# Optimization experiments

Hardware: AMD Instinct MI355X
Metric: run time of the kernel (lower is better)

Reference implementation:

```python
import jax, jax.numpy as jnp
import numpy as np

TOP_K = 8
NUM_EXPERTS = 32
CAPACITY = 1024


def setup_inputs() -> dict:
    key = jax.random.key(0)
    k1, k2, k3, k4 = jax.random.split(key, 4)
    B, S, H, E, F = 2, 1024, 1024, NUM_EXPERTS, 768
    return {
        "hidden_states": jax.random.normal(k1, (B, S, H), dtype=jnp.float32),
        "gate_weight": jax.random.normal(k2, (E, H), dtype=jnp.float32) * 0.02,
        "gate_up_proj": jax.random.normal(k3, (E, 2 * F, H), dtype=jnp.float32) * 0.02,
        "down_proj": jax.random.normal(k4, (E, H, F), dtype=jnp.float32) * 0.02,
    }


def reference(hidden_states, gate_weight, gate_up_proj, down_proj):
    B, S, H = hidden_states.shape
    E = gate_weight.shape[0]
    N = B * S
    x = hidden_states.reshape(N, H)

    # Router: fp32 softmax, top-k, renormalize (norm_topk_prob=True)
    logits = x @ gate_weight.T                                   # [N, E]
    probs = jax.nn.softmax(logits.astype(jnp.float32), axis=-1)
    topw, topi = jax.lax.top_k(probs, TOP_K)                     # [N, K]
    topw = topw / topw.sum(-1, keepdims=True)
    topw = topw.astype(x.dtype)

    # Flatten token-slot view (matches repeat_interleave ordering)
    flat_e = topi.reshape(-1)                                    # [N*K] int
    flat_w = topw.reshape(-1)                                    # [N*K]
    flat_x = jnp.repeat(x, TOP_K, axis=0)                        # [N*K, H]

    # Position of each slot within its expert (stable order, like stable argsort)
    oh = jax.nn.one_hot(flat_e, E, dtype=jnp.int32)              # [N*K, E]
    pos = (jnp.cumsum(oh, axis=0) * oh).sum(-1) - 1              # [N*K]

    # Dispatch into per-expert buffers [E, C, H]; grouped GEMMs; gather back
    buf = jnp.zeros((E, CAPACITY, H), x.dtype).at[flat_e, pos].set(flat_x, mode="drop")
    gu = jnp.einsum("ech,efh->ecf", buf, gate_up_proj)           # [E, C, 2F]
    gate, up = jnp.split(gu, 2, axis=-1)
    h = jax.nn.silu(gate) * up                                   # [E, C, F]
    eo = jnp.einsum("ecf,ehf->ech", h, down_proj)                # [E, C, H]
    tok_out = eo.at[flat_e, pos].get(mode="fill", fill_value=0)  # [N*K, H]

    out = (tok_out * flat_w[:, None]).reshape(N, TOP_K, H).sum(1)
    return out.reshape(B, S, H)
```

## Files before the change

kernel.cpp:

```cpp
#include <hip/hip_runtime.h>
#include <stdint.h>
#include <math.h>

#define NTOK  2048
#define HDIM  1024
#define FDIM  768
#define NEXP  32
#define TOPK  8
#define CAP   1024

typedef __attribute__((ext_vector_type(8))) short short8;
typedef __attribute__((ext_vector_type(4))) float f32x4;

__device__ __forceinline__ short f2bf(float f) {
  union { float f; uint32_t u; } c; c.f = f;
  uint32_t u = c.u;
  u += 0x7fffu + ((u >> 16) & 1u);
  return (short)(u >> 16);
}

__device__ __forceinline__ short8 pack8(float4 a, float4 b) {
  short8 r;
  r[0] = f2bf(a.x); r[1] = f2bf(a.y); r[2] = f2bf(a.z); r[3] = f2bf(a.w);
  r[4] = f2bf(b.x); r[5] = f2bf(b.y); r[6] = f2bf(b.z); r[7] = f2bf(b.w);
  return r;
}

__device__ __forceinline__ void gload16(const short* g, short* l) {
  __builtin_amdgcn_global_load_lds(
      (__attribute__((address_space(1))) uint32_t*)g,
      (__attribute__((address_space(3))) uint32_t*)l, 16, 0, 0);
}

__global__ __launch_bounds__(256) void cvt_kern(
    const float* __restrict__ gup, const float* __restrict__ dwn,
    short* __restrict__ gupb, short* __restrict__ dwnb) {
  const size_t NG8 = (size_t)NEXP * 2 * FDIM * HDIM / 8;
  const size_t ND8 = (size_t)NEXP * HDIM * FDIM / 8;
  const size_t tid = (size_t)blockIdx.x * 256 + threadIdx.x;
  const size_t stride = (size_t)gridDim.x * 256;
  for (size_t i = tid; i < NG8; i += stride) {
    const float4 a = *(const float4*)(gup + i * 8);
    const float4 b = *(const float4*)(gup + i * 8 + 4);
    *(short8*)(gupb + i * 8) = pack8(a, b);
  }
  for (size_t i = tid; i < ND8; i += stride) {
    const float4 a = *(const float4*)(dwn + i * 8);
    const float4 b = *(const float4*)(dwn + i * 8 + 4);
    *(short8*)(dwnb + i * 8) = pack8(a, b);
  }
}

__global__ __launch_bounds__(256) void router_kern(
    const float* __restrict__ x, const float* __restrict__ gw,
    int* __restrict__ cnt, int* __restrict__ slot_tok,
    float* __restrict__ slot_w, short* __restrict__ xb) {
  const int n0 = blockIdx.x * 8;
  const int t  = threadIdx.x;
  __shared__ float ls[8][32];

  const int e = t >> 3;
  const int j = t & 7;
  float acc[8];
#pragma unroll
  for (int i = 0; i < 8; ++i) acc[i] = 0.f;
  const float* gwe = gw + (size_t)e * HDIM;
  for (int i = 0; i < 128; ++i) {
    const int k = j + 8 * i;
    const float gv = gwe[k];
#pragma unroll
    for (int tok = 0; tok < 8; ++tok)
      acc[tok] += gv * x[(size_t)(n0 + tok) * HDIM + k];
  }
#pragma unroll
  for (int tok = 0; tok < 8; ++tok) {
    float v = acc[tok];
    v += __shfl_xor(v, 1); v += __shfl_xor(v, 2); v += __shfl_xor(v, 4);
    if (j == 0) ls[tok][e] = v;
  }
  __syncthreads();

  if (t < 8) {
    const int n = n0 + t;
    float lv[32];
#pragma unroll
    for (int i = 0; i < 32; ++i) lv[i] = ls[t][i];
    int   idx[TOPK];
    float val[TOPK];
    for (int kk = 0; kk < TOPK; ++kk) {
      float best = -INFINITY; int bi = 0;
      for (int i = 0; i < 32; ++i)
        if (lv[i] > best) { best = lv[i]; bi = i; }
      val[kk] = best; idx[kk] = bi; lv[bi] = -INFINITY;
    }
    const float m = val[0];
    float w[TOPK]; float wsum = 0.f;
    for (int kk = 0; kk < TOPK; ++kk) { w[kk] = __expf(val[kk] - m); wsum += w[kk]; }
    const float inv = 1.f / wsum;
    for (int kk = 0; kk < TOPK; ++kk) {
      const int ee = idx[kk];
      const int pos = atomicAdd(&cnt[ee], 1);
      if (pos < CAP) {
        slot_tok[ee * CAP + pos] = n * TOPK + kk;
        slot_w[ee * CAP + pos]   = w[kk] * inv;
      }
    }
  }

  const size_t base = (size_t)n0 * HDIM;
  for (int i = t; i < 8 * HDIM; i += 256)
    xb[base + i] = f2bf(x[base + i]);
}

__global__ __launch_bounds__(256) void gemm1_kern(
    const short* __restrict__ xb, const short* __restrict__ gupb,
    const int* __restrict__ cnt, const int* __restrict__ slot_tok,
    short* __restrict__ hbuf) {
  const int id  = blockIdx.x;
  const int xcd = id & 7;
  const int idx = id >> 3;
  const int e   = xcd + 8 * (idx / 96);
  const int w96 = idx % 96;
  const int f0  = (w96 % 12) * 64;
  const int r0  = (w96 / 12) * 128;

  const int mcnt = min(cnt[e], CAP);
  if (r0 >= mcnt) return;

  __shared__ short As[2][128 * 32];
  __shared__ short Bg[2][64 * 32];
  __shared__ short Bu[2][64 * 32];

  const int t = threadIdx.x;
  const int wave = t >> 6, lane = t & 63;

  const int la0 = wave * 128 + lane;
  const int la1 = la0 + 64;
  const int arow0 = la0 >> 2, aseg0 = la0 & 3;
  const int arow1 = la1 >> 2, aseg1 = la1 & 3;
  int tok0 = 0, tok1 = 0;
  if (r0 + arow0 < mcnt) tok0 = slot_tok[e * CAP + r0 + arow0] >> 3;
  if (r0 + arow1 < mcnt) tok1 = slot_tok[e * CAP + r0 + arow1] >> 3;
  const short* aSrc0 = xb + (size_t)tok0 * HDIM + aseg0 * 8;
  const short* aSrc1 = xb + (size_t)tok1 * HDIM + aseg1 * 8;

  const int brow = t >> 2, bseg = t & 3;
  const short* gSrc = gupb + ((size_t)e * 1536 + f0 + brow) * HDIM + bseg * 8;
  const short* uSrc = gupb + ((size_t)e * 1536 + 768 + f0 + brow) * HDIM + bseg * 8;

  const int wm = (wave & 1) * 64, wf = (wave >> 1) * 32;
  const int lrow = lane & 15, lk = (lane >> 4) * 8;

  f32x4 accg[4][2], accu[4][2];
#pragma unroll
  for (int a = 0; a < 4; ++a)
#pragma unroll
    for (int b = 0; b < 2; ++b) {
      accg[a][b] = (f32x4){0.f, 0.f, 0.f, 0.f};
      accu[a][b] = (f32x4){0.f, 0.f, 0.f, 0.f};
    }

  auto STAGE = [&](int b, int kb) {
    gload16(aSrc0 + kb, &As[b][wave * 1024]);
    gload16(aSrc1 + kb, &As[b][wave * 1024 + 512]);
    gload16(gSrc + kb,  &Bg[b][wave * 512]);
    gload16(uSrc + kb,  &Bu[b][wave * 512]);
  };

  auto COMPUTE = [&](int b) {
    short8 af[4], bg[2], bu[2];
#pragma unroll
    for (int mt = 0; mt < 4; ++mt)
      af[mt] = *(const short8*)&As[b][(wm + mt * 16 + lrow) * 32 + lk];
#pragma unroll
    for (int nt = 0; nt < 2; ++nt) {
      bg[nt] = *(const short8*)&Bg[b][(wf + nt * 16 + lrow) * 32 + lk];
      bu[nt] = *(const short8*)&Bu[b][(wf + nt * 16 + lrow) * 32 + lk];
    }
#pragma unroll
    for (int mt = 0; mt < 4; ++mt)
#pragma unroll
      for (int nt = 0; nt < 2; ++nt) {
        accg[mt][nt] = __builtin_amdgcn_mfma_f32_16x16x32_bf16(af[mt], bg[nt], accg[mt][nt], 0, 0, 0);
        accu[mt][nt] = __builtin_amdgcn_mfma_f32_16x16x32_bf16(af[mt], bu[nt], accu[mt][nt], 0, 0, 0);
      }
  };

  STAGE(0, 0);
  __syncthreads();
  int cur = 0;
  for (int kb = 32; kb < HDIM; kb += 32) {
    STAGE(cur ^ 1, kb);
    COMPUTE(cur);
    __syncthreads();
    cur ^= 1;
  }
  COMPUTE(cur);

#pragma unroll
  for (int mt = 0; mt < 4; ++mt)
#pragma unroll
    for (int rr = 0; rr < 4; ++rr) {
      const int pos = r0 + wm + mt * 16 + (lane >> 4) * 4 + rr;
      if (pos < mcnt) {
#pragma unroll
        for (int nt = 0; nt < 2; ++nt) {
          const float g = accg[mt][nt][rr];
          const float u = accu[mt][nt][rr];
          const float hv = (g / (1.f + __expf(-g))) * u;
          hbuf[((size_t)e * CAP + pos) * FDIM + f0 + wf + nt * 16 + (lane & 15)] = f2bf(hv);
        }
      }
    }
}

__global__ __launch_bounds__(256) void gemm2_kern(
    const short* __restrict__ hbuf, const short* __restrict__ dwnb,
    const int* __restrict__ cnt, const int* __restrict__ slot_tok,
    const float* __restrict__ slot_w, float* __restrict__ slot_out) {
  const int id  = blockIdx.x;
  const int xcd = id & 7;
  const int idx = id >> 3;
  const int e   = xcd + 8 * (idx >> 6);
  const int w64 = idx & 63;
  const int n0  = (w64 & 7) * 128;
  const int r0  = (w64 >> 3) * 128;

  const int mcnt = min(cnt[e], CAP);
  if (r0 >= mcnt) return;

  __shared__ short As[2][128 * 32];
  __shared__ short Bs[2][128 * 32];

  const int t = threadIdx.x;
  const int wave = t >> 6, lane = t & 63;

  const int l0 = wave * 128 + lane;
  const int l1 = l0 + 64;
  const int ar0 = l0 >> 2, as0 = l0 & 3;
  const int ar1 = l1 >> 2, as1 = l1 & 3;
  const short* aSrc0 = hbuf + ((size_t)e * CAP + r0 + ar0) * FDIM + as0 * 8;
  const short* aSrc1 = hbuf + ((size_t)e * CAP + r0 + ar1) * FDIM + as1 * 8;
  const short* bSrc0 = dwnb + ((size_t)e * HDIM + n0 + ar0) * FDIM + as0 * 8;
  const short* bSrc1 = dwnb + ((size_t)e * HDIM + n0 + ar1) * FDIM + as1 * 8;

  const int wm = (wave & 1) * 64, wn = (wave >> 1) * 64;
  const int lrow = lane & 15, lk = (lane >> 4) * 8;

  f32x4 acc[4][4];
#pragma unroll
  for (int a = 0; a < 4; ++a)
#pragma unroll
    for (int b = 0; b < 4; ++b) acc[a][b] = (f32x4){0.f, 0.f, 0.f, 0.f};

  auto STAGE = [&](int b, int kb) {
    gload16(aSrc0 + kb, &As[b][wave * 1024]);
    gload16(aSrc1 + kb, &As[b][wave * 1024 + 512]);
    gload16(bSrc0 + kb, &Bs[b][wave * 1024]);
    gload16(bSrc1 + kb, &Bs[b][wave * 1024 + 512]);
  };

  auto COMPUTE = [&](int b) {
    short8 af[4], bf[4];
#pragma unroll
    for (int i = 0; i < 4; ++i) {
      af[i] = *(const short8*)&As[b][(wm + i * 16 + lrow) * 32 + lk];
      bf[i] = *(const short8*)&Bs[b][(wn + i * 16 + lrow) * 32 + lk];
    }
#pragma unroll
    for (int mt = 0; mt < 4; ++mt)
#pragma unroll
      for (int nt = 0; nt < 4; ++nt)
        acc[mt][nt] = __builtin_amdgcn_mfma_f32_16x16x32_bf16(af[mt], bf[nt], acc[mt][nt], 0, 0, 0);
  };

  STAGE(0, 0);
  __syncthreads();
  int cur = 0;
  for (int kb = 32; kb < FDIM; kb += 32) {
    STAGE(cur ^ 1, kb);
    COMPUTE(cur);
    __syncthreads();
    cur ^= 1;
  }
  COMPUTE(cur);

#pragma unroll
  for (int mt = 0; mt < 4; ++mt)
#pragma unroll
    for (int rr = 0; rr < 4; ++rr) {
      const int pos = r0 + wm + mt * 16 + (lane >> 4) * 4 + rr;
      if (pos < mcnt) {
        const int s = slot_tok[e * CAP + pos];
        const float w = slot_w[e * CAP + pos];
#pragma unroll
        for (int nt = 0; nt < 4; ++nt)
          slot_out[(size_t)s * HDIM + n0 + wn + nt * 16 + (lane & 15)] = w * acc[mt][nt][rr];
      }
    }
}

__global__ __launch_bounds__(256) void gather_kern(
    const float* __restrict__ so, float* __restrict__ out) {
  const int n = blockIdx.x;
  const int c = threadIdx.x * 4;
  float4 a = make_float4(0.f, 0.f, 0.f, 0.f);
#pragma unroll
  for (int k = 0; k < TOPK; ++k) {
    const float4 v = *(const float4*)&so[((size_t)(n * TOPK + k)) * HDIM + c];
    a.x += v.x; a.y += v.y; a.z += v.z; a.w += v.w;
  }
  *(float4*)&out[(size_t)n * HDIM + c] = a;
}

extern "C" void kernel_launch(void* const* d_in, const int* in_sizes, int n_in,
                              void* d_out, int out_size, void* d_ws, size_t ws_size,
                              hipStream_t stream) {
  const float* x   = (const float*)d_in[0];
  const float* gw  = (const float*)d_in[1];
  const float* gup = (const float*)d_in[2];
  const float* dwn = (const float*)d_in[3];
  float* out = (float*)d_out;

  char* ws = (char*)d_ws;
  int*   cnt      = (int*)(ws + 0);
  int*   slot_tok = (int*)(ws + 1024);
  float* slot_w   = (float*)(ws + 1024 + 131072);
  short* xb       = (short*)(ws + 524288);
  short* hbuf     = (short*)(ws + 4718592);
  short* gupb     = (short*)(ws + 55050240);
  short* dwnb     = (short*)(ws + 155713536);
  float* slot_out = (float*)(ws + 206045184);

  hipMemsetAsync(cnt, 0, 1024, stream);
  router_kern<<<NTOK / 8, 256, 0, stream>>>(x, gw, cnt, slot_tok, slot_w, xb);
  cvt_kern<<<4096, 256, 0, stream>>>(gup, dwn, gupb, dwnb);
  gemm1_kern<<<3072, 256, 0, stream>>>(xb, gupb, cnt, slot_tok, hbuf);
  gemm2_kern<<<2048, 256, 0, stream>>>(hbuf, dwnb, cnt, slot_tok, slot_w, slot_out);
  gather_kern<<<NTOK, 256, 0, stream>>>(slot_out, out);
}
```

Before: 603.7 us.

## Fuse fp32-to-bf16 weight conversion into grouped GEMM tile loads

Removes the separate kernel that converted all expert weights to bf16 each call. The GEMMs instead load fp32 weight tiles into registers and pack them to bf16 when writing shared memory, overlapped with the MFMA compute on the other buffer. This avoids a full-weight write and re-read pass, at the cost of reading twice as many weight bytes per tile, repeated across row blocks. It also replaces asynchronous LDS-direct loads with register-staged loads.

```diff
diff --git a/kernel.cpp b/kernel.cpp
--- a/kernel.cpp
+++ b/kernel.cpp
@@ -30,25 +30,6 @@
   __builtin_amdgcn_global_load_lds(
       (__attribute__((address_space(1))) uint32_t*)g,
       (__attribute__((address_space(3))) uint32_t*)l, 16, 0, 0);
-}
-
-__global__ __launch_bounds__(256) void cvt_kern(
-    const float* __restrict__ gup, const float* __restrict__ dwn,
-    short* __restrict__ gupb, short* __restrict__ dwnb) {
-  const size_t NG8 = (size_t)NEXP * 2 * FDIM * HDIM / 8;
-  const size_t ND8 = (size_t)NEXP * HDIM * FDIM / 8;
-  const size_t tid = (size_t)blockIdx.x * 256 + threadIdx.x;
-  const size_t stride = (size_t)gridDim.x * 256;
-  for (size_t i = tid; i < NG8; i += stride) {
-    const float4 a = *(const float4*)(gup + i * 8);
-    const float4 b = *(const float4*)(gup + i * 8 + 4);
-    *(short8*)(gupb + i * 8) = pack8(a, b);
-  }
-  for (size_t i = tid; i < ND8; i += stride) {
-    const float4 a = *(const float4*)(dwn + i * 8);
-    const float4 b = *(const float4*)(dwn + i * 8 + 4);
-    *(short8*)(dwnb + i * 8) = pack8(a, b);
-  }
 }
 
 __global__ __launch_bounds__(256) void router_kern(
@@ -113,7 +94,7 @@
 }
 
 __global__ __launch_bounds__(256) void gemm1_kern(
-    const short* __restrict__ xb, const short* __restrict__ gupb,
+    const short* __restrict__ xb, const float* __restrict__ gup,
     const int* __restrict__ cnt, const int* __restrict__ slot_tok,
     short* __restrict__ hbuf) {
   const int id  = blockIdx.x;
@@ -145,8 +126,8 @@
   const short* aSrc1 = xb + (size_t)tok1 * HDIM + aseg1 * 8;
 
   const int brow = t >> 2, bseg = t & 3;
-  const short* gSrc = gupb + ((size_t)e * 1536 + f0 + brow) * HDIM + bseg * 8;
-  const short* uSrc = gupb + ((size_t)e * 1536 + 768 + f0 + brow) * HDIM + bseg * 8;
+  const float* gSrcF = gup + ((size_t)(e * 1536 + f0 + brow)) * HDIM + bseg * 8;
+  const float* uSrcF = gup + ((size_t)(e * 1536 + 768 + f0 + brow)) * HDIM + bseg * 8;
 
   const int wm = (wave & 1) * 64, wf = (wave >> 1) * 32;
   const int lrow = lane & 15, lk = (lane >> 4) * 8;
@@ -160,11 +141,20 @@
       accu[a][b] = (f32x4){0.f, 0.f, 0.f, 0.f};
     }
 
-  auto STAGE = [&](int b, int kb) {
+  float4 g0, g1, u0, u1;
+
+  auto STAGE_LOAD = [&](int b, int kb) {
     gload16(aSrc0 + kb, &As[b][wave * 1024]);
     gload16(aSrc1 + kb, &As[b][wave * 1024 + 512]);
-    gload16(gSrc + kb,  &Bg[b][wave * 512]);
-    gload16(uSrc + kb,  &Bu[b][wave * 512]);
+    g0 = *(const float4*)(gSrcF + kb);
+    g1 = *(const float4*)(gSrcF + kb + 4);
+    u0 = *(const float4*)(uSrcF + kb);
+    u1 = *(const float4*)(uSrcF + kb + 4);
+  };
+
+  auto STAGE_WRITE = [&](int b) {
+    *(short8*)&Bg[b][t * 8] = pack8(g0, g1);
+    *(short8*)&Bu[b][t * 8] = pack8(u0, u1);
   };
 
   auto COMPUTE = [&](int b) {
@@ -186,12 +176,14 @@
       }
   };
 
-  STAGE(0, 0);
+  STAGE_LOAD(0, 0);
+  STAGE_WRITE(0);
   __syncthreads();
   int cur = 0;
   for (int kb = 32; kb < HDIM; kb += 32) {
-    STAGE(cur ^ 1, kb);
+    STAGE_LOAD(cur ^ 1, kb);
     COMPUTE(cur);
+    STAGE_WRITE(cur ^ 1);
     __syncthreads();
     cur ^= 1;
   }
@@ -215,7 +207,7 @@
 }
 
 __global__ __launch_bounds__(256) void gemm2_kern(
-    const short* __restrict__ hbuf, const short* __restrict__ dwnb,
+    const short* __restrict__ hbuf, const float* __restrict__ dwn,
     const int* __restrict__ cnt, const int* __restrict__ slot_tok,
     const float* __restrict__ slot_w, float* __restrict__ slot_out) {
   const int id  = blockIdx.x;
@@ -241,8 +233,8 @@
   const int ar1 = l1 >> 2, as1 = l1 & 3;
   const short* aSrc0 = hbuf + ((size_t)e * CAP + r0 + ar0) * FDIM + as0 * 8;
   const short* aSrc1 = hbuf + ((size_t)e * CAP + r0 + ar1) * FDIM + as1 * 8;
-  const short* bSrc0 = dwnb + ((size_t)e * HDIM + n0 + ar0) * FDIM + as0 * 8;
-  const short* bSrc1 = dwnb + ((size_t)e * HDIM + n0 + ar1) * FDIM + as1 * 8;
+  const float* bSrcF0 = dwn + ((size_t)(e * HDIM + n0 + ar0)) * FDIM + as0 * 8;
+  const float* bSrcF1 = dwn + ((size_t)(e * HDIM + n0 + ar1)) * FDIM + as1 * 8;
 
   const int wm = (wave & 1) * 64, wn = (wave >> 1) * 64;
   const int lrow = lane & 15, lk = (lane >> 4) * 8;
@@ -253,11 +245,20 @@
 #pragma unroll
     for (int b = 0; b < 4; ++b) acc[a][b] = (f32x4){0.f, 0.f, 0.f, 0.f};
 
-  auto STAGE = [&](int b, int kb) {
+  float4 b00, b01, b10, b11;
+
+  auto STAGE_LOAD = [&](int b, int kb) {
     gload16(aSrc0 + kb, &As[b][wave * 1024]);
     gload16(aSrc1 + kb, &As[b][wave * 1024 + 512]);
-    gload16(bSrc0 + kb, &Bs[b][wave * 1024]);
-    gload16(bSrc1 + kb, &Bs[b][wave * 1024 + 512]);
+    b00 = *(const float4*)(bSrcF0 + kb);
+    b01 = *(const float4*)(bSrcF0 + kb + 4);
+    b10 = *(const float4*)(bSrcF1 + kb);
+    b11 = *(const float4*)(bSrcF1 + kb + 4);
+  };
+
+  auto STAGE_WRITE = [&](int b) {
+    *(short8*)&Bs[b][l0 * 8] = pack8(b00, b01);
+    *(short8*)&Bs[b][l1 * 8] = pack8(b10, b11);
   };
 
   auto COMPUTE = [&](int b) {
@@ -274,12 +275,14 @@
         acc[mt][nt] = __builtin_amdgcn_mfma_f32_16x16x32_bf16(af[mt], bf[nt], acc[mt][nt], 0, 0, 0);
   };
 
-  STAGE(0, 0);
+  STAGE_LOAD(0, 0);
+  STAGE_WRITE(0);
   __syncthreads();
   int cur = 0;
   for (int kb = 32; kb < FDIM; kb += 32) {
-    STAGE(cur ^ 1, kb);
+    STAGE_LOAD(cur ^ 1, kb);
     COMPUTE(cur);
+    STAGE_WRITE(cur ^ 1);
     __syncthreads();
     cur ^= 1;
   }
@@ -328,14 +331,11 @@
   float* slot_w   = (float*)(ws + 1024 + 131072);
   short* xb       = (short*)(ws + 524288);
   short* hbuf     = (short*)(ws + 4718592);
-  short* gupb     = (short*)(ws + 55050240);
-  short* dwnb     = (short*)(ws + 155713536);
-  float* slot_out = (float*)(ws + 206045184);
+  float* slot_out = (float*)(ws + 55050240);
 
   hipMemsetAsync(cnt, 0, 1024, stream);
   router_kern<<<NTOK / 8, 256, 0, stream>>>(x, gw, cnt, slot_tok, slot_w, xb);
-  cvt_kern<<<4096, 256, 0, stream>>>(gup, dwn, gupb, dwnb);
-  gemm1_kern<<<3072, 256, 0, stream>>>(xb, gupb, cnt, slot_tok, hbuf);
-  gemm2_kern<<<2048, 256, 0, stream>>>(hbuf, dwnb, cnt, slot_tok, slot_w, slot_out);
+  gemm1_kern<<<3072, 256, 0, stream>>>(xb, gup, cnt, slot_tok, hbuf);
+  gemm2_kern<<<2048, 256, 0, stream>>>(hbuf, dwn, cnt, slot_tok, slot_w, slot_out);
   gather_kern<<<NTOK, 256, 0, stream>>>(slot_out, out);
 }
```

Result: faster. 562.4 us (-6.8%).
